# Performance work log

Hardware: AMD Instinct MI355X
Metric: run time of the kernel (lower is better)

Reference implementation:

```python
import jax, jax.numpy as jnp
import numpy as np

HEADS = 8
EMBED = 768
FFN = 4 * EMBED
LN_EPS = 1e-5


def _layernorm(x, g, b):
    m = jnp.mean(x, axis=-1, keepdims=True)
    v = jnp.var(x, axis=-1, keepdims=True)
    return (x - m) * jax.lax.rsqrt(v + LN_EPS) * g + b


def _attention(xn, ctx, Wq, Wkv, Wo, bo, mask):
    # xn: [B, N, C], ctx: [B, M, C], mask: [B, 1, N, M] bool (True = keep)
    B, N, C = xn.shape
    d = C // HEADS
    q = (xn @ Wq).reshape(B, N, HEADS, d).transpose(0, 2, 1, 3)          # b h i d
    k, v = jnp.split(ctx @ Wkv, 2, axis=-1)
    k = k.reshape(B, -1, HEADS, d).transpose(0, 2, 1, 3)                 # b h j d
    v = v.reshape(B, -1, HEADS, d).transpose(0, 2, 1, 3)
    sim = jnp.einsum('bhid,bhjd->bhij', q, k) * (d ** -0.5)
    sim = jnp.where(mask, sim, -jnp.finfo(sim.dtype).max)
    attn = jax.nn.softmax(sim, axis=-1)
    out = jnp.einsum('bhij,bhjd->bhid', attn, v)
    out = out.transpose(0, 2, 1, 3).reshape(B, N, C)
    return out @ Wo + bo


def _block(x, c, effect_lengths, us_rate,
           Wq1, Wkv1, Wo1, bo1, Wq2, Wkv2, Wo2, bo2,
           g1, b1, g2, b2, g4, b4, gc, bc, Wf1, bf1, Wf2, bf2):
    B, L, C = x.shape
    S = c.shape[1]
    el = effect_lengths * us_rate                                        # [B]
    i = jnp.arange(L)
    j_self = jnp.arange(L)
    j_cross = jnp.arange(S)
    # ragged per-sample masks, broadcast over heads: [B, 1, L, L] / [B, 1, L, S]
    mask1 = ((i[None, :, None] < el[:, None, None]) &
             (j_self[None, None, :] < el[:, None, None]))[:, None]
    mask2 = ((i[None, :, None] < el[:, None, None]) &
             (j_cross[None, None, :] < effect_lengths[:, None, None]))[:, None]

    xn = _layernorm(x, g1, b1)
    x = x + _attention(xn, xn, Wq1, Wkv1, Wo1, bo1, mask1)
    xn = _layernorm(x, g2, b2)
    cn = _layernorm(c, gc, bc)
    x = x + _attention(xn, cn, Wq2, Wkv2, Wo2, bo2, mask2)
    xn = _layernorm(x, g4, b4)
    x = x + (jax.nn.gelu(xn @ Wf1 + bf1, approximate=False) @ Wf2 + bf2)
    return x


def setup_inputs() -> dict:
    key = jax.random.key(0)
    ks = jax.random.split(key, 20)
    B, S, US = 8, 512, 2
    L = S * US
    s = 0.02
    inp = {
        'x': jax.random.normal(ks[0], (B, L, EMBED), jnp.float32),
        'c': jax.random.normal(ks[1], (B, S, EMBED), jnp.float32),
        'effect_lengths': jax.random.randint(ks[2], (B,), 1, S + 1),
        'us_rate': US,
        'Wq1': jax.random.normal(ks[3], (EMBED, EMBED), jnp.float32) * s,
        'Wkv1': jax.random.normal(ks[4], (EMBED, 2 * EMBED), jnp.float32) * s,
        'Wo1': jax.random.normal(ks[5], (EMBED, EMBED), jnp.float32) * s,
        'bo1': jnp.zeros((EMBED,), jnp.float32),
        'Wq2': jax.random.normal(ks[6], (EMBED, EMBED), jnp.float32) * s,
        'Wkv2': jax.random.normal(ks[7], (EMBED, 2 * EMBED), jnp.float32) * s,
        'Wo2': jax.random.normal(ks[8], (EMBED, EMBED), jnp.float32) * s,
        'bo2': jnp.zeros((EMBED,), jnp.float32),
        'g1': jnp.ones((EMBED,), jnp.float32), 'b1': jnp.zeros((EMBED,), jnp.float32),
        'g2': jnp.ones((EMBED,), jnp.float32), 'b2': jnp.zeros((EMBED,), jnp.float32),
        'g4': jnp.ones((EMBED,), jnp.float32), 'b4': jnp.zeros((EMBED,), jnp.float32),
        'gc': jnp.ones((EMBED,), jnp.float32), 'bc': jnp.zeros((EMBED,), jnp.float32),
        'Wf1': jax.random.normal(ks[9], (EMBED, FFN), jnp.float32) * s,
        'bf1': jnp.zeros((FFN,), jnp.float32),
        'Wf2': jax.random.normal(ks[10], (FFN, EMBED), jnp.float32) * s,
        'bf2': jnp.zeros((EMBED,), jnp.float32),
    }
    return inp


def reference(x, c, effect_lengths, us_rate,
              Wq1, Wkv1, Wo1, bo1, Wq2, Wkv2, Wo2, bo2,
              g1, b1, g2, b2, g4, b4, gc, bc, Wf1, bf1, Wf2, bf2):
    return _block(x, c, effect_lengths, us_rate,
                  Wq1, Wkv1, Wo1, bo1, Wq2, Wkv2, Wo2, bo2,
                  g1, b1, g2, b2, g4, b4, gc, bc, Wf1, bf1, Wf2, bf2)
```

## Files before the change

kernel.cpp:

```cpp
#include <hip/hip_runtime.h>
#include <math.h>

#define EMBED 768
#define HEADS 8
#define HDIM  96
#define NEG_MASK (-1.0e30f)

typedef unsigned short u16;
typedef unsigned int   u32;

typedef __attribute__((ext_vector_type(4))) float f32x4;
typedef __attribute__((ext_vector_type(8))) short short8;

__device__ __forceinline__ float bf2f(u16 u) {
    return __uint_as_float(((u32)u) << 16);
}
__device__ __forceinline__ u16 f2bf(float f) {
    u32 x = __float_as_uint(f);
    u32 r = (x + 0x7fffu + ((x >> 16) & 1u)) >> 16;
    return (u16)r;
}
__device__ __forceinline__ void unpack2(u32 w, float& lo, float& hi) {
    lo = __uint_as_float(w << 16);
    hi = __uint_as_float(w & 0xffff0000u);
}
__device__ __forceinline__ float wget(const void* p, size_t i, int wf) {
    return wf ? ((const float*)p)[i] : bf2f(((const u16*)p)[i]);
}
__device__ __forceinline__ int bswz(int r, int g) {
    return ((g ^ (r & 3) ^ ((r >> 2) & 3) ^ ((r >> 4) & 3)) << 3);
}

__global__ __launch_bounds__(64) void detect_kernel(const u16* __restrict__ x,
                                                    const int* __restrict__ el,
                                                    const int* __restrict__ usp,
                                                    int* __restrict__ blk) {
    int lane = threadIdx.x;
    int cnt = 0;
    for (int i = lane; i < 4096; i += 64) {
        u32 e = (x[i] >> 7) & 0xFFu;
        if (e >= 0xC0u) cnt++;
    }
#pragma unroll
    for (int off = 32; off > 0; off >>= 1) cnt += __shfl_xor(cnt, off, 64);
    if (lane == 0) {
        blk[0] = (cnt > 32) ? 1 : 0;
        bool i64 = (el[1] == 0) && (el[3] == 0) && (el[5] == 0) && (el[7] == 0);
        for (int b = 0; b < 8; b++) blk[1 + b] = i64 ? el[2 * b] : el[b];
        blk[9] = usp[0];
    }
}

__global__ void wire_to_f32(const void* __restrict__ in, size_t ioff,
                            float* __restrict__ out, int n,
                            const int* __restrict__ blk) {
    int i = blockIdx.x * blockDim.x + threadIdx.x;
    int wf = blk[0];
    if (i < n) out[i] = wget(in, ioff + (size_t)i, wf);
}
__global__ void wire_copy(const void* __restrict__ in, void* __restrict__ out,
                          int n, const int* __restrict__ blk) {
    int i = blockIdx.x * blockDim.x + threadIdx.x;
    int wf = blk[0];
    if (i < n) {
        if (wf) ((float*)out)[i] = ((const float*)in)[i];
        else    ((u16*)out)[i]   = ((const u16*)in)[i];
    }
}
__global__ void f32_to_out(const float* __restrict__ in, void* __restrict__ out,
                           size_t ooff, int n, const int* __restrict__ blk) {
    int i = blockIdx.x * blockDim.x + threadIdx.x;
    int wf = blk[0];
    if (i < n) {
        if (wf) ((float*)out)[ooff + i] = in[i];
        else    ((u16*)out)[ooff + i]   = f2bf(in[i]);
    }
}

__global__ __launch_bounds__(256) void wtrans_kernel(const void* __restrict__ W, size_t woff,
                                                     int ldw, int K,
                                                     u16* __restrict__ WT,
                                                     const int* __restrict__ blk) {
    __shared__ u16 T[64][65];
    int wf = blk[0];
    int n0 = blockIdx.x * 64, k0 = blockIdx.y * 64;
    int tid = threadIdx.x;
    int tr = tid >> 4, tc4 = (tid & 15) * 4;
#pragma unroll
    for (int i = 0; i < 4; i++) {
        int k = tr + i * 16;
        if (wf) {
            const float* src = (const float*)W + woff + (size_t)(k0 + k) * ldw + n0 + tc4;
            float4 f = *(const float4*)src;
            T[tc4 + 0][k] = f2bf(f.x); T[tc4 + 1][k] = f2bf(f.y);
            T[tc4 + 2][k] = f2bf(f.z); T[tc4 + 3][k] = f2bf(f.w);
        } else {
            const u16* src = (const u16*)W + woff + (size_t)(k0 + k) * ldw + n0 + tc4;
            uint2 u = *(const uint2*)src;
            T[tc4 + 0][k] = (u16)(u.x & 0xffffu); T[tc4 + 1][k] = (u16)(u.x >> 16);
            T[tc4 + 2][k] = (u16)(u.y & 0xffffu); T[tc4 + 3][k] = (u16)(u.y >> 16);
        }
    }
    __syncthreads();
#pragma unroll
    for (int i = 0; i < 4; i++) {
        int n = tr + i * 16;
        u32 w0 = (u32)T[n][tc4 + 0] | ((u32)T[n][tc4 + 1] << 16);
        u32 w1 = (u32)T[n][tc4 + 2] | ((u32)T[n][tc4 + 3] << 16);
        *(uint2*)(WT + (size_t)(n0 + n) * K + k0 + tc4) = make_uint2(w0, w1);
    }
}

__global__ __launch_bounds__(256) void ln_kernel(const void* __restrict__ in,
                                                 size_t ioff, int sel,
                                                 const void* __restrict__ g,
                                                 const void* __restrict__ b,
                                                 u16* __restrict__ out,
                                                 const int* __restrict__ blk) {
    int wf = blk[0];
    int row = blockIdx.x, tid = threadIdx.x;
    size_t base = ioff + (size_t)row * EMBED;
    float v[3];
#pragma unroll
    for (int e = 0; e < 3; e++) {
        size_t idx = base + tid + e * 256;
        v[e] = (sel == 0) ? ((const float*)in)[idx] : wget(in, idx, wf);
    }
    float s = v[0] + v[1] + v[2];
    float q = v[0] * v[0] + v[1] * v[1] + v[2] * v[2];
#pragma unroll
    for (int off = 32; off > 0; off >>= 1) {
        s += __shfl_xor(s, off, 64);
        q += __shfl_xor(q, off, 64);
    }
    __shared__ float sb[8];
    int wid = tid >> 6, lane = tid & 63;
    if (lane == 0) { sb[wid] = s; sb[4 + wid] = q; }
    __syncthreads();
    if (tid == 0) {
        sb[0] = sb[0] + sb[1] + sb[2] + sb[3];
        sb[4] = sb[4] + sb[5] + sb[6] + sb[7];
    }
    __syncthreads();
    float mean = sb[0] * (1.0f / EMBED);
    float var  = sb[4] * (1.0f / EMBED) - mean * mean;
    float rs   = rsqrtf(var + 1e-5f);
    size_t obase = (size_t)row * EMBED;
#pragma unroll
    for (int e = 0; e < 3; e++) {
        int col = tid + e * 256;
        out[obase + col] = f2bf((v[e] - mean) * rs * wget(g, col, wf) + wget(b, col, wf));
    }
}

__global__ __launch_bounds__(256) void gemm_kernel(const u16* __restrict__ A,
                                                   const void* __restrict__ W,
                                                   size_t woff, int ldw,
                                                   const void* __restrict__ bias, int boff,
                                                   void* __restrict__ Cv, size_t coff,
                                                   int M, int N, int K, int flags,
                                                   int tcmode, const int* __restrict__ blk) {
    __shared__ float As[16][64];
    __shared__ float Bs[16][64];
    int wf = blk[0];
    int tid = threadIdx.x;
    int tx = tid & 15, ty = tid >> 4;
    int row0 = blockIdx.y * 64, col0 = blockIdx.x * 64;
    float acc[4][4] = {};
    int ar = tid >> 2, ac4 = tid & 3;
    int br = tid >> 4, bc4 = tid & 15;

    for (int kb = 0; kb < K; kb += 16) {
        {
            uint2 u = *(const uint2*)(A + (size_t)(row0 + ar) * K + kb + ac4 * 4);
            float a0, a1, a2, a3;
            unpack2(u.x, a0, a1); unpack2(u.y, a2, a3);
            As[ac4 * 4 + 0][ar] = a0; As[ac4 * 4 + 1][ar] = a1;
            As[ac4 * 4 + 2][ar] = a2; As[ac4 * 4 + 3][ar] = a3;
        }
        {
            size_t off = woff + (size_t)(kb + br) * ldw + col0 + bc4 * 4;
            if (wf) {
                float4 u = *(const float4*)((const float*)W + off);
                Bs[br][bc4 * 4 + 0] = u.x; Bs[br][bc4 * 4 + 1] = u.y;
                Bs[br][bc4 * 4 + 2] = u.z; Bs[br][bc4 * 4 + 3] = u.w;
            } else {
                uint2 u = *(const uint2*)((const u16*)W + off);
                float b0, b1, b2, b3;
                unpack2(u.x, b0, b1); unpack2(u.y, b2, b3);
                Bs[br][bc4 * 4 + 0] = b0; Bs[br][bc4 * 4 + 1] = b1;
                Bs[br][bc4 * 4 + 2] = b2; Bs[br][bc4 * 4 + 3] = b3;
            }
        }
        __syncthreads();
#pragma unroll
        for (int kk = 0; kk < 16; kk++) {
            float4 a = *(const float4*)&As[kk][ty * 4];
            float4 b = *(const float4*)&Bs[kk][tx * 4];
            float av[4] = {a.x, a.y, a.z, a.w};
            float bv[4] = {b.x, b.y, b.z, b.w};
#pragma unroll
            for (int i = 0; i < 4; i++)
#pragma unroll
                for (int j = 0; j < 4; j++)
                    acc[i][j] += av[i] * bv[j];
        }
        __syncthreads();
    }

#pragma unroll
    for (int i = 0; i < 4; i++) {
        int m = row0 + ty * 4 + i;
#pragma unroll
        for (int j = 0; j < 4; j++) {
            int n = col0 + tx * 4 + j;
            float v = acc[i][j];
            if (flags & 1) v += wget(bias, boff + n, wf);
            if (flags & 2) v = 0.5f * v * (1.0f + erff(v * 0.70710678118654752f));
            size_t idx = coff + (size_t)m * N + n;
            if (tcmode == 0) {
                ((float*)Cv)[idx] += v;
            } else if (tcmode == 1) {
                ((u16*)Cv)[idx] = f2bf(v);
            } else {
                if (wf) ((float*)Cv)[idx] += v;
                else { u16* p = (u16*)Cv; p[idx] = f2bf(v + bf2f(p[idx])); }
            }
        }
    }
}

__global__ __launch_bounds__(256) void gemm_mfma(const u16* __restrict__ A,
                                                 const void* __restrict__ W,
                                                 size_t woff, int ldw,
                                                 const void* __restrict__ bias, int boff,
                                                 void* __restrict__ Cv, size_t coff,
                                                 int M, int N, int K, int flags,
                                                 int tcmode, const int* __restrict__ blk) {
    __shared__ __align__(16) u16 As[128 * 32];
    __shared__ __align__(16) u16 Bs[128 * 32];
    int wf = blk[0];
    int tid = threadIdx.x;
    int wave = tid >> 6, lane = tid & 63;
    int x = lane & 15, g = lane >> 4;
    int wm = wave >> 1, wn = wave & 1;
    int row0 = blockIdx.y * 128, col0 = blockIdx.x * 128;

    int ar  = tid >> 1, ah = tid & 1;
    int bk  = tid >> 3, bn0 = (tid & 7) * 16;

    f32x4 acc[4][4];
#pragma unroll
    for (int i = 0; i < 4; i++)
#pragma unroll
        for (int j = 0; j < 4; j++) acc[i][j] = (f32x4){0.f, 0.f, 0.f, 0.f};

    for (int kb = 0; kb < K; kb += 32) {
        {
            const u16* asrc = A + (size_t)(row0 + ar) * K + kb + ah * 16;
            uint4 a0 = *(const uint4*)asrc;
            uint4 a1 = *(const uint4*)(asrc + 8);
            *(uint4*)&As[ar * 32 + bswz(ar, ah * 2 + 0)] = a0;
            *(uint4*)&As[ar * 32 + bswz(ar, ah * 2 + 1)] = a1;
        }
        {
            u16 bv[16];
            if (wf) {
                const float* wsrc = (const float*)W + woff + (size_t)(kb + bk) * ldw + col0 + bn0;
#pragma unroll
                for (int i = 0; i < 16; i += 4) {
                    float4 f = *(const float4*)(wsrc + i);
                    bv[i + 0] = f2bf(f.x); bv[i + 1] = f2bf(f.y);
                    bv[i + 2] = f2bf(f.z); bv[i + 3] = f2bf(f.w);
                }
            } else {
                const u16* wsrc = (const u16*)W + woff + (size_t)(kb + bk) * ldw + col0 + bn0;
                ((uint4*)bv)[0] = *(const uint4*)wsrc;
                ((uint4*)bv)[1] = *(const uint4*)(wsrc + 8);
            }
            int kg = bk >> 3, kl = bk & 7;
#pragma unroll
            for (int i = 0; i < 16; i++)
                Bs[(bn0 + i) * 32 + bswz(bn0 + i, kg) + kl] = bv[i];
        }
        __syncthreads();

        short8 af[4], bf[4];
#pragma unroll
        for (int mt = 0; mt < 4; mt++) {
            int r = wm * 64 + mt * 16 + x;
            af[mt] = *(const short8*)&As[r * 32 + bswz(r, g)];
        }
#pragma unroll
        for (int nt = 0; nt < 4; nt++) {
            int n = wn * 64 + nt * 16 + x;
            bf[nt] = *(const short8*)&Bs[n * 32 + bswz(n, g)];
        }
#pragma unroll
        for (int mt = 0; mt < 4; mt++)
#pragma unroll
            for (int nt = 0; nt < 4; nt++)
                acc[mt][nt] = __builtin_amdgcn_mfma_f32_16x16x32_bf16(af[mt], bf[nt], acc[mt][nt], 0, 0, 0);
        __syncthreads();
    }

#pragma unroll
    for (int mt = 0; mt < 4; mt++) {
#pragma unroll
        for (int nt = 0; nt < 4; nt++) {
#pragma unroll
            for (int r = 0; r < 4; r++) {
                int m = row0 + wm * 64 + mt * 16 + g * 4 + r;
                int n = col0 + wn * 64 + nt * 16 + x;
                float v = acc[mt][nt][r];
                if (flags & 1) v += wget(bias, boff + n, wf);
                if (flags & 2) v = 0.5f * v * (1.0f + erff(v * 0.70710678118654752f));
                size_t idx = coff + (size_t)m * N + n;
                if (tcmode == 0) {
                    ((float*)Cv)[idx] += v;
                } else if (tcmode == 1) {
                    ((u16*)Cv)[idx] = f2bf(v);
                } else {
                    if (wf) ((float*)Cv)[idx] += v;
                    else { u16* p = (u16*)Cv; p[idx] = f2bf(v + bf2f(p[idx])); }
                }
            }
        }
    }
}

__global__ __launch_bounds__(256) void gemm_mfma_t(const u16* __restrict__ A,
                                                   const u16* __restrict__ BT,
                                                   const void* __restrict__ bias, int boff,
                                                   void* __restrict__ Cv, size_t coff,
                                                   int M, int N, int K, int flags,
                                                   int tcmode, const int* __restrict__ blk) {
    __shared__ __align__(16) u16 As[2][128 * 32];
    __shared__ __align__(16) u16 Bs[2][128 * 32];
    int wf = blk[0];
    int tid = threadIdx.x;
    int wave = tid >> 6, lane = tid & 63;
    int x = lane & 15, g = lane >> 4;
    int wm = wave >> 1, wn = wave & 1;
    int row0 = blockIdx.y * 128, col0 = blockIdx.x * 128;
    int KS = gridDim.z, kz = blockIdx.z;
    int Kc = K / KS;

    int sr = tid >> 1;
    int sg = (tid & 1) * 2;
    const u16* aptr = A  + (size_t)(row0 + sr) * K + kz * Kc + sg * 8;
    const u16* bptr = BT + (size_t)(col0 + sr) * K + kz * Kc + sg * 8;
    int wo0 = sr * 32 + bswz(sr, sg);
    int wo1 = sr * 32 + bswz(sr, sg + 1);

    int ra[4], rb[4];
#pragma unroll
    for (int t = 0; t < 4; t++) {
        int r = wm * 64 + t * 16 + x;
        int n = wn * 64 + t * 16 + x;
        ra[t] = r * 32 + bswz(r, g);
        rb[t] = n * 32 + bswz(n, g);
    }

    f32x4 acc[4][4];
#pragma unroll
    for (int i = 0; i < 4; i++)
#pragma unroll
        for (int j = 0; j < 4; j++) acc[i][j] = (f32x4){0.f, 0.f, 0.f, 0.f};

    int nsteps = Kc >> 5;

    {
        uint4 a0 = *(const uint4*)aptr, a1 = *(const uint4*)(aptr + 8);
        uint4 b0 = *(const uint4*)bptr, b1 = *(const uint4*)(bptr + 8);
        *(uint4*)&As[0][wo0] = a0; *(uint4*)&As[0][wo1] = a1;
        *(uint4*)&Bs[0][wo0] = b0; *(uint4*)&Bs[0][wo1] = b1;
    }
    uint4 s0a0 = {}, s0a1 = {}, s0b0 = {}, s0b1 = {};
    uint4 s1a0 = {}, s1a1 = {}, s1b0 = {}, s1b1 = {};
    if (nsteps > 1) {
        aptr += 32; bptr += 32;
        s1a0 = *(const uint4*)aptr; s1a1 = *(const uint4*)(aptr + 8);
        s1b0 = *(const uint4*)bptr; s1b1 = *(const uint4*)(bptr + 8);
    }
    __syncthreads();

#define GSTEP(S, LA0, LA1, LB0, LB1, WA0, WA1, WB0, WB1)                          \
    {                                                                             \
        if ((S) + 2 < nsteps) {                                                   \
            aptr += 32; bptr += 32;                                               \
            LA0 = *(const uint4*)aptr; LA1 = *(const uint4*)(aptr + 8);           \
            LB0 = *(const uint4*)bptr; LB1 = *(const uint4*)(bptr + 8);           \
        }                                                                         \
        short8 af[4], bfr[4];                                                     \
        _Pragma("unroll")                                                         \
        for (int mt = 0; mt < 4; mt++)                                            \
            af[mt] = *(const short8*)&As[(S) & 1][ra[mt]];                        \
        _Pragma("unroll")                                                         \
        for (int nt = 0; nt < 4; nt++)                                            \
            bfr[nt] = *(const short8*)&Bs[(S) & 1][rb[nt]];                       \
        _Pragma("unroll")                                                         \
        for (int mt = 0; mt < 4; mt++)                                            \
            _Pragma("unroll")                                                     \
            for (int nt = 0; nt < 4; nt++)                                        \
                acc[mt][nt] = __builtin_amdgcn_mfma_f32_16x16x32_bf16(            \
                    af[mt], bfr[nt], acc[mt][nt], 0, 0, 0);                       \
        if ((S) + 1 < nsteps) {                                                   \
            int nb = (((S) & 1) ^ 1);                                             \
            *(uint4*)&As[nb][wo0] = WA0; *(uint4*)&As[nb][wo1] = WA1;             \
            *(uint4*)&Bs[nb][wo0] = WB0; *(uint4*)&Bs[nb][wo1] = WB1;             \
            __syncthreads();                                                      \
        }                                                                         \
    }

    for (int s = 0; s < nsteps; s += 2) {
        GSTEP(s, s0a0, s0a1, s0b0, s0b1, s1a0, s1a1, s1b0, s1b1);
        if (s + 1 < nsteps)
            GSTEP(s + 1, s1a0, s1a1, s1b0, s1b1, s0a0, s0a1, s0b0, s0b1);
    }
#undef GSTEP

    bool kz0 = (kz == 0);
#pragma unroll
    for (int mt = 0; mt < 4; mt++) {
#pragma unroll
        for (int nt = 0; nt < 4; nt++) {
#pragma unroll
            for (int r = 0; r < 4; r++) {
                int m = row0 + wm * 64 + mt * 16 + g * 4 + r;
                int n = col0 + wn * 64 + nt * 16 + x;
                float v = acc[mt][nt][r];
                if ((flags & 1) && kz0) v += wget(bias, boff + n, wf);
                if (flags & 2) v = 0.5f * v * (1.0f + erff(v * 0.70710678118654752f));
                size_t idx = coff + (size_t)m * N + n;
                if (tcmode == 0) {
                    if (KS > 1) atomicAdd(&((float*)Cv)[idx], v);
                    else        ((float*)Cv)[idx] += v;
                } else if (tcmode == 1) {
                    ((u16*)Cv)[idx] = f2bf(v);
                } else {
                    if (wf) ((float*)Cv)[idx] += v;
                    else { u16* p = (u16*)Cv; p[idx] = f2bf(v + bf2f(p[idx])); }
                }
            }
        }
    }
}

__global__ __launch_bounds__(256) void attn_kernel(const u16* __restrict__ Q,
                                                   const u16* __restrict__ K,
                                                   const u16* __restrict__ V,
                                                   u16* __restrict__ AO,
                                                   int ldq, int ldk, int ldv, int ldo,
                                                   size_t qss, size_t kss, size_t oss,
                                                   const int* __restrict__ blk,
                                                   int bfix, int Lk, int is_self) {
    int bz   = (bfix < 0) ? blockIdx.z : 0;
    int bidx = (bfix < 0) ? blockIdx.z : bfix;
    const u16* Qp = Q + (size_t)bz * qss;
    const u16* Kp = K + (size_t)bz * kss;
    const u16* Vp = V + (size_t)bz * kss;
    u16* AOp = AO + (size_t)bz * oss;

    int hoff = blockIdx.y * HDIM;
    int i0 = blockIdx.x * 64;
    int tid = threadIdx.x;
    int wave = tid >> 6, lane = tid & 63;
    int x = lane & 15, g = lane >> 4;

    int elb = blk[1 + bidx];
    int el_q = elb * blk[9];
    int el_k = is_self ? el_q : elb;

    __shared__ __align__(16) u16 Ks[64 * 96];
    __shared__ __align__(16) u16 Vs[96 * 64];
    __shared__ __align__(16) u16 Ps[4][16 * 72];

    short8 qf[3];
    {
        const u16* qrow = Qp + (size_t)(i0 + wave * 16 + x) * ldq + hoff;
#pragma unroll
        for (int kc = 0; kc < 3; kc++)
            qf[kc] = *(const short8*)(qrow + kc * 32 + g * 8);
    }

    const f32x4 zero4 = {0.f, 0.f, 0.f, 0.f};
    f32x4 o[6];
#pragma unroll
    for (int dt = 0; dt < 6; dt++) o[dt] = zero4;
    float m[4], l[4];
#pragma unroll
    for (int r = 0; r < 4; r++) { m[r] = NEG_MASK; l[r] = 0.f; }

    bool qok[4];
#pragma unroll
    for (int r = 0; r < 4; r++) qok[r] = (i0 + wave * 16 + g * 4 + r) < el_q;

    const float scale = 0.10206207261596576f;
    u16* pw = &Ps[wave][0];

    for (int kt0 = 0; kt0 < Lk; kt0 += 64) {
#pragma unroll
        for (int t = 0; t < 3; t++) {
            int idx = tid + t * 256;
            int j = idx / 12, c = idx % 12;
            *(uint4*)&Ks[j * 96 + c * 8] =
                *(const uint4*)(Kp + (size_t)(kt0 + j) * ldk + hoff + c * 8);
            uint4 vu = *(const uint4*)(Vp + (size_t)(kt0 + j) * ldv + hoff + c * 8);
            u16 vv[8] = {(u16)(vu.x & 0xffffu), (u16)(vu.x >> 16),
                         (u16)(vu.y & 0xffffu), (u16)(vu.y >> 16),
                         (u16)(vu.z & 0xffffu), (u16)(vu.z >> 16),
                         (u16)(vu.w & 0xffffu), (u16)(vu.w >> 16)};
            int jb = j >> 3, jl = j & 7;
#pragma unroll
            for (int ii = 0; ii < 8; ii++) {
                int d = c * 8 + ii;
                int sb = jb ^ (d & 7) ^ ((d >> 3) & 7);
                Vs[d * 64 + sb * 8 + jl] = vv[ii];
            }
        }
        __syncthreads();

        f32x4 st[4];
#pragma unroll
        for (int t = 0; t < 4; t++) {
            f32x4 acc = zero4;
#pragma unroll
            for (int kc = 0; kc < 3; kc++) {
                short8 kf = *(const short8*)&Ks[(t * 16 + x) * 96 + kc * 32 + g * 8];
                acc = __builtin_amdgcn_mfma_f32_16x16x32_bf16(qf[kc], kf, acc, 0, 0, 0);
            }
            st[t] = acc;
        }

#pragma unroll
        for (int t = 0; t < 4; t++) {
            bool kv_ok = (kt0 + t * 16 + x) < el_k;
#pragma unroll
            for (int r = 0; r < 4; r++)
                st[t][r] = (kv_ok && qok[r]) ? st[t][r] * scale : NEG_MASK;
        }

        float al[4];
#pragma unroll
        for (int r = 0; r < 4; r++) {
            float rm = fmaxf(fmaxf(st[0][r], st[1][r]), fmaxf(st[2][r], st[3][r]));
            rm = fmaxf(rm, __shfl_xor(rm, 1, 64));
            rm = fmaxf(rm, __shfl_xor(rm, 2, 64));
            rm = fmaxf(rm, __shfl_xor(rm, 4, 64));
            rm = fmaxf(rm, __shfl_xor(rm, 8, 64));
            float mn = fmaxf(m[r], rm);
            al[r] = __expf(m[r] - mn);
            m[r] = mn;
            l[r] *= al[r];
        }
#pragma unroll
        for (int dt = 0; dt < 6; dt++)
#pragma unroll
            for (int r = 0; r < 4; r++) o[dt][r] *= al[r];

#pragma unroll
        for (int t = 0; t < 4; t++)
#pragma unroll
            for (int r = 0; r < 4; r++) {
                float p = __expf(st[t][r] - m[r]);
                l[r] += p;
                pw[(g * 4 + r) * 72 + t * 16 + x] = f2bf(p);
            }

#pragma unroll
        for (int kc = 0; kc < 2; kc++) {
            short8 pf = *(const short8*)&pw[x * 72 + kc * 32 + g * 8];
#pragma unroll
            for (int dt = 0; dt < 6; dt++) {
                int d = dt * 16 + x;
                int sb = (kc * 4 + g) ^ (d & 7) ^ ((d >> 3) & 7);
                short8 vf = *(const short8*)&Vs[d * 64 + sb * 8];
                o[dt] = __builtin_amdgcn_mfma_f32_16x16x32_bf16(pf, vf, o[dt], 0, 0, 0);
            }
        }
        __syncthreads();
    }

    float inv[4];
#pragma unroll
    for (int r = 0; r < 4; r++) {
        float lr = l[r];
        lr += __shfl_xor(lr, 1, 64);
        lr += __shfl_xor(lr, 2, 64);
        lr += __shfl_xor(lr, 4, 64);
        lr += __shfl_xor(lr, 8, 64);
        inv[r] = 1.0f / lr;
    }
#pragma unroll
    for (int dt = 0; dt < 6; dt++)
#pragma unroll
        for (int r = 0; r < 4; r++) {
            size_t ob = (size_t)(i0 + wave * 16 + g * 4 + r) * ldo + hoff + dt * 16 + x;
            AOp[ob] = f2bf(o[dt][r] * inv[r]);
        }
}

extern "C" void kernel_launch(void* const* d_in, const int* in_sizes, int n_in,
                              void* d_out, int out_size, void* d_ws, size_t ws_size,
                              hipStream_t stream) {
    const void* x    = d_in[0];
    const void* c    = d_in[1];
    const int* el    = (const int*)d_in[2];
    const int* us    = (const int*)d_in[3];
    const void* Wq1  = d_in[4];
    const void* Wkv1 = d_in[5];
    const void* Wo1  = d_in[6];
    const void* bo1  = d_in[7];
    const void* Wq2  = d_in[8];
    const void* Wkv2 = d_in[9];
    const void* Wo2  = d_in[10];
    const void* bo2  = d_in[11];
    const void* g1 = d_in[12]; const void* b1 = d_in[13];
    const void* g2 = d_in[14]; const void* b2 = d_in[15];
    const void* g4 = d_in[16]; const void* b4 = d_in[17];
    const void* gc = d_in[18]; const void* bc = d_in[19];
    const void* Wf1 = d_in[20]; const void* bf1 = d_in[21];
    const void* Wf2 = d_in[22]; const void* bf2 = d_in[23];

    const int B = 8, S = 512, L = 1024, C = EMBED;
    const int NX = B * L * C;
    const size_t RL = (size_t)L * C;
    const size_t RS = (size_t)S * C;

    char* ws = (char*)d_ws;
    int*  blk = (int*)ws;
    dim3 blkd(256);

    bool tierA = ws_size >= (size_t)88080448;
    bool tierB = !tierA && ws_size >= (size_t)33030208;

    detect_kernel<<<1, 64, 0, stream>>>((const u16*)x, el, us, blk);

    if (tierA) {
        float* X  = (float*)(ws + 64);
        u16*   XN = (u16*)(ws + 25165888);
        u16*   WT = (u16*)(ws + 37748800);
        char*  P  = ws + 47185984;
        u16* Qb   = (u16*)P;
        u16* KVb  = (u16*)(P + 12582912);
        u16* CNb  = (u16*)P;
        u16* KV2b = (u16*)(P + 6291456);
        u16* Q2b  = (u16*)(P + 18874368);
        u16* Hh   = (u16*)P;
        const size_t WTq = 0, WTkv = 589824, WTo = 1769472;
        const size_t WTf1 = 0, WTf2 = 2359296;

        wire_to_f32<<<(NX + 255) / 256, blkd, 0, stream>>>(x, 0, X, NX, blk);

        wtrans_kernel<<<dim3(12, 12), blkd, 0, stream>>>(Wq1, 0, C, C, WT + WTq, blk);
        wtrans_kernel<<<dim3(24, 12), blkd, 0, stream>>>(Wkv1, 0, 2 * C, C, WT + WTkv, blk);
        wtrans_kernel<<<dim3(12, 12), blkd, 0, stream>>>(Wo1, 0, C, C, WT + WTo, blk);

        ln_kernel<<<B * L, blkd, 0, stream>>>(X, 0, 0, g1, b1, XN, blk);
        gemm_mfma_t<<<dim3(6, 64, 1), blkd, 0, stream>>>(XN, WT + WTq, nullptr, 0, Qb, 0, B * L, C, C, 0, 1, blk);
        gemm_mfma_t<<<dim3(12, 64, 1), blkd, 0, stream>>>(XN, WT + WTkv, nullptr, 0, KVb, 0, B * L, 2 * C, C, 0, 1, blk);
        attn_kernel<<<dim3(16, 8, 8), blkd, 0, stream>>>(Qb, KVb, KVb + C, Qb, C, 2 * C, 2 * C, C,
                                                         RL, (size_t)L * 2 * C, RL, blk, -1, L, 1);
        gemm_mfma_t<<<dim3(6, 64, 2), blkd, 0, stream>>>(Qb, WT + WTo, bo1, 0, X, 0, B * L, C, C, 1, 0, blk);

        wtrans_kernel<<<dim3(12, 12), blkd, 0, stream>>>(Wq2, 0, C, C, WT + WTq, blk);
        wtrans_kernel<<<dim3(24, 12), blkd, 0, stream>>>(Wkv2, 0, 2 * C, C, WT + WTkv, blk);
        wtrans_kernel<<<dim3(12, 12), blkd, 0, stream>>>(Wo2, 0, C, C, WT + WTo, blk);

        ln_kernel<<<B * L, blkd, 0, stream>>>(X, 0, 0, g2, b2, XN, blk);
        ln_kernel<<<B * S, blkd, 0, stream>>>(c, 0, 2, gc, bc, CNb, blk);
        gemm_mfma_t<<<dim3(12, 32, 1), blkd, 0, stream>>>(CNb, WT + WTkv, nullptr, 0, KV2b, 0, B * S, 2 * C, C, 0, 1, blk);
        gemm_mfma_t<<<dim3(6, 64, 1), blkd, 0, stream>>>(XN, WT + WTq, nullptr, 0, Q2b, 0, B * L, C, C, 0, 1, blk);
        attn_kernel<<<dim3(16, 8, 8), blkd, 0, stream>>>(Q2b, KV2b, KV2b + C, Q2b, C, 2 * C, 2 * C, C,
                                                         RL, (size_t)S * 2 * C, RL, blk, -1, S, 0);
        gemm_mfma_t<<<dim3(6, 64, 2), blkd, 0, stream>>>(Q2b, WT + WTo, bo2, 0, X, 0, B * L, C, C, 1, 0, blk);

        wtrans_kernel<<<dim3(48, 12), blkd, 0, stream>>>(Wf1, 0, 4 * C, C, WT + WTf1, blk);
        wtrans_kernel<<<dim3(12, 48), blkd, 0, stream>>>(Wf2, 0, C, 4 * C, WT + WTf2, blk);

        ln_kernel<<<B * L, blkd, 0, stream>>>(X, 0, 0, g4, b4, XN, blk);
        for (int h = 0; h < 2; h++) {
            size_t ro = (size_t)h * 4096 * C;
            gemm_mfma_t<<<dim3(24, 32, 1), blkd, 0, stream>>>(XN + ro, WT + WTf1, bf1, 0, Hh, 0, 4096, 4 * C, C, 1 | 2, 1, blk);
            gemm_mfma_t<<<dim3(6, 32, 2), blkd, 0, stream>>>(Hh, WT + WTf2, bf2, 0, X, ro, 4096, C, 4 * C, 1, 0, blk);
        }

        f32_to_out<<<(NX + 255) / 256, blkd, 0, stream>>>(X, d_out, 0, NX, blk);
    } else if (tierB) {
        float* X  = (float*)(ws + 64);
        u16*   XN = (u16*)(ws + 64 + 25165824);
        char*  P  = ws + 64 + 25165824 + 1572864;
        u16* Qb   = (u16*)P;
        u16* KVb  = (u16*)(P + 1572864);
        u16* AOb  = (u16*)(P + 4718592);
        u16* CNb  = (u16*)P;
        u16* KV2b = (u16*)(P + 786432);
        u16* Q2b  = (u16*)(P + 2359296);
        u16* AO2b = (u16*)(P + 3932160);
        u16* Hb   = (u16*)P;

        wire_to_f32<<<(NX + 255) / 256, blkd, 0, stream>>>(x, 0, X, NX, blk);

        for (int b = 0; b < B; b++) {
            size_t ro = (size_t)b * RL;
            ln_kernel<<<L, blkd, 0, stream>>>(X, ro, 0, g1, b1, XN, blk);
            gemm_mfma<<<dim3(6, 8), blkd, 0, stream>>>(XN, Wq1, 0, C, nullptr, 0, Qb, 0, L, C, C, 0, 1, blk);
            gemm_mfma<<<dim3(12, 8), blkd, 0, stream>>>(XN, Wkv1, 0, 2 * C, nullptr, 0, KVb, 0, L, 2 * C, C, 0, 1, blk);
            attn_kernel<<<dim3(16, 8), blkd, 0, stream>>>(Qb, KVb, KVb + C, AOb, C, 2 * C, 2 * C, C, 0, 0, 0, blk, b, L, 1);
            gemm_mfma<<<dim3(6, 8), blkd, 0, stream>>>(AOb, Wo1, 0, C, bo1, 0, X, ro, L, C, C, 1, 0, blk);

            ln_kernel<<<L, blkd, 0, stream>>>(X, ro, 0, g2, b2, XN, blk);
            ln_kernel<<<S, blkd, 0, stream>>>(c, (size_t)b * RS, 2, gc, bc, CNb, blk);
            gemm_mfma<<<dim3(12, 4), blkd, 0, stream>>>(CNb, Wkv2, 0, 2 * C, nullptr, 0, KV2b, 0, S, 2 * C, C, 0, 1, blk);
            gemm_mfma<<<dim3(6, 8), blkd, 0, stream>>>(XN, Wq2, 0, C, nullptr, 0, Q2b, 0, L, C, C, 0, 1, blk);
            attn_kernel<<<dim3(16, 8), blkd, 0, stream>>>(Q2b, KV2b, KV2b + C, AO2b, C, 2 * C, 2 * C, C, 0, 0, 0, blk, b, S, 0);
            gemm_mfma<<<dim3(6, 8), blkd, 0, stream>>>(AO2b, Wo2, 0, C, bo2, 0, X, ro, L, C, C, 1, 0, blk);

            ln_kernel<<<L, blkd, 0, stream>>>(X, ro, 0, g4, b4, XN, blk);
            gemm_mfma<<<dim3(24, 8), blkd, 0, stream>>>(XN, Wf1, 0, 4 * C, bf1, 0, Hb, 0, L, 4 * C, C, 1 | 2, 1, blk);
            gemm_mfma<<<dim3(6, 8), blkd, 0, stream>>>(Hb, Wf2, 0, C, bf2, 0, X, ro, L, C, 4 * C, 1, 0, blk);
        }
        f32_to_out<<<(NX + 255) / 256, blkd, 0, stream>>>(X, d_out, 0, NX, blk);
    } else {
        u16*  XN  = (u16*)(ws + 64);
        u16*  CNb = (u16*)(ws + 64 + 1572864);
        char* P2  = ws + 64 + 1572864 + 786432;
        u16* Qp  = (u16*)P2;
        u16* Kp  = (u16*)(P2 + 393216);
        u16* Vp  = (u16*)(P2 + 786432);
        u16* AOp = (u16*)(P2 + 1179648);
        u16* Hc  = (u16*)P2;

        wire_copy<<<(NX + 255) / 256, blkd, 0, stream>>>(x, d_out, NX, blk);

        for (int b = 0; b < B; b++) {
            size_t ro = (size_t)b * RL;

            ln_kernel<<<L, blkd, 0, stream>>>(d_out, ro, 2, g1, b1, XN, blk);
            for (int p = 0; p < 4; p++) {
                int h = 2 * p;
                gemm_kernel<<<dim3(3, 16), blkd, 0, stream>>>(XN, Wq1, (size_t)h * 96, C, nullptr, 0, Qp, 0, L, 192, C, 0, 1, blk);
                gemm_kernel<<<dim3(3, 16), blkd, 0, stream>>>(XN, Wkv1, (size_t)h * 96, 2 * C, nullptr, 0, Kp, 0, L, 192, C, 0, 1, blk);
                gemm_kernel<<<dim3(3, 16), blkd, 0, stream>>>(XN, Wkv1, (size_t)(C + h * 96), 2 * C, nullptr, 0, Vp, 0, L, 192, C, 0, 1, blk);
                attn_kernel<<<dim3(16, 2), blkd, 0, stream>>>(Qp, Kp, Vp, AOp, 192, 192, 192, 192, 0, 0, 0, blk, b, L, 1);
                gemm_kernel<<<dim3(12, 16), blkd, 0, stream>>>(AOp, Wo1, (size_t)h * 96 * C, C, bo1, 0, d_out, ro, L, C, 192, (p == 0) ? 1 : 0, 3, blk);
            }
            ln_kernel<<<L, blkd, 0, stream>>>(d_out, ro, 2, g2, b2, XN, blk);
            ln_kernel<<<S, blkd, 0, stream>>>(c, (size_t)b * RS, 2, gc, bc, CNb, blk);
            for (int p = 0; p < 4; p++) {
                int h = 2 * p;
                gemm_kernel<<<dim3(3, 16), blkd, 0, stream>>>(XN, Wq2, (size_t)h * 96, C, nullptr, 0, Qp, 0, L, 192, C, 0, 1, blk);
                gemm_kernel<<<dim3(3, 8), blkd, 0, stream>>>(CNb, Wkv2, (size_t)h * 96, 2 * C, nullptr, 0, Kp, 0, S, 192, C, 0, 1, blk);
                gemm_kernel<<<dim3(3, 8), blkd, 0, stream>>>(CNb, Wkv2, (size_t)(C + h * 96), 2 * C, nullptr, 0, Vp, 0, S, 192, C, 0, 1, blk);
                attn_kernel<<<dim3(16, 2), blkd, 0, stream>>>(Qp, Kp, Vp, AOp, 192, 192, 192, 192, 0, 0, 0, blk, b, S, 0);
                gemm_kernel<<<dim3(12, 16), blkd, 0, stream>>>(AOp, Wo2, (size_t)h * 96 * C, C, bo2, 0, d_out, ro, L, C, 192, (p == 0) ? 1 : 0, 3, blk);
            }
            ln_kernel<<<L, blkd, 0, stream>>>(d_out, ro, 2, g4, b4, XN, blk);
            for (int ch = 0; ch < 4; ch++) {
                gemm_kernel<<<dim3(12, 16), blkd, 0, stream>>>(XN, Wf1, (size_t)ch * C, 4 * C, bf1, ch * C, Hc, 0, L, C, C, 1 | 2, 1, blk);
                gemm_kernel<<<dim3(12, 16), blkd, 0, stream>>>(Hc, Wf2, (size_t)ch * C * C, C, bf2, 0, d_out, ro, L, C, C, (ch == 0) ? 1 : 0, 3, blk);
            }
        }
    }
}
```

Baseline: 924.0 us.

## Shrink GEMM M-tile to 64, add LDS-only barrier, skip masked attention tiles

The MFMA GEMM tile shrinks from 128x128 to 64x128, doubling the grid for better CU occupancy, and the out-projection GEMMs drop split-K. The __syncthreads is replaced by a barrier that waits only on LDS counters, so in-flight global prefetches are not drained. The attention kernel trims the key loop to the valid effective length for fully valid query tiles, and skips QK loads and MFMAs for fully masked query tiles while keeping the V path. These cut wasted compute on masked regions and improve GEMM parallelism, at the cost of lower per-block reuse in the GEMM.

After: 850.8 us. 7.9% less time.

```diff
diff --git a/kernel.cpp b/kernel.cpp
--- a/kernel.cpp
+++ b/kernel.cpp
@@ -29,6 +29,12 @@
 }
 __device__ __forceinline__ int bswz(int r, int g) {
     return ((g ^ (r & 3) ^ ((r >> 2) & 3) ^ ((r >> 4) & 3)) << 3);
+}
+__device__ __forceinline__ void lds_barrier() {
+    __builtin_amdgcn_sched_barrier(0);
+    asm volatile("s_waitcnt lgkmcnt(0)" ::: "memory");
+    __builtin_amdgcn_s_barrier();
+    __builtin_amdgcn_sched_barrier(0);
 }
 
 __global__ __launch_bounds__(64) void detect_kernel(const u16* __restrict__ x,
@@ -335,99 +341,100 @@
                                                    void* __restrict__ Cv, size_t coff,
                                                    int M, int N, int K, int flags,
                                                    int tcmode, const int* __restrict__ blk) {
-    __shared__ __align__(16) u16 As[2][128 * 32];
+    __shared__ __align__(16) u16 As[2][64 * 32];
     __shared__ __align__(16) u16 Bs[2][128 * 32];
     int wf = blk[0];
     int tid = threadIdx.x;
     int wave = tid >> 6, lane = tid & 63;
     int x = lane & 15, g = lane >> 4;
     int wm = wave >> 1, wn = wave & 1;
-    int row0 = blockIdx.y * 128, col0 = blockIdx.x * 128;
+    int row0 = blockIdx.y * 64, col0 = blockIdx.x * 128;
     int KS = gridDim.z, kz = blockIdx.z;
     int Kc = K / KS;
 
-    int sr = tid >> 1;
-    int sg = (tid & 1) * 2;
-    const u16* aptr = A  + (size_t)(row0 + sr) * K + kz * Kc + sg * 8;
-    const u16* bptr = BT + (size_t)(col0 + sr) * K + kz * Kc + sg * 8;
-    int wo0 = sr * 32 + bswz(sr, sg);
-    int wo1 = sr * 32 + bswz(sr, sg + 1);
-
-    int ra[4], rb[4];
-#pragma unroll
-    for (int t = 0; t < 4; t++) {
-        int r = wm * 64 + t * 16 + x;
-        int n = wn * 64 + t * 16 + x;
-        ra[t] = r * 32 + bswz(r, g);
-        rb[t] = n * 32 + bswz(n, g);
-    }
-
-    f32x4 acc[4][4];
-#pragma unroll
-    for (int i = 0; i < 4; i++)
+    int ar = tid >> 2, ac = tid & 3;
+    const u16* aptr = A + (size_t)(row0 + ar) * K + kz * Kc + ac * 8;
+    int awo = ar * 32 + bswz(ar, ac);
+    int br = tid >> 1, bh = tid & 1;
+    const u16* bptr = BT + (size_t)(col0 + br) * K + kz * Kc + bh * 16;
+    int bwo0 = br * 32 + bswz(br, 2 * bh);
+    int bwo1 = br * 32 + bswz(br, 2 * bh + 1);
+
+    int ra[2], rb[4];
+#pragma unroll
+    for (int mt = 0; mt < 2; mt++) {
+        int r = wm * 32 + mt * 16 + x;
+        ra[mt] = r * 32 + bswz(r, g);
+    }
+#pragma unroll
+    for (int nt = 0; nt < 4; nt++) {
+        int n = wn * 64 + nt * 16 + x;
+        rb[nt] = n * 32 + bswz(n, g);
+    }
+
+    f32x4 acc[2][4];
+#pragma unroll
+    for (int i = 0; i < 2; i++)
 #pragma unroll
         for (int j = 0; j < 4; j++) acc[i][j] = (f32x4){0.f, 0.f, 0.f, 0.f};
 
     int nsteps = Kc >> 5;
 
-    {
-        uint4 a0 = *(const uint4*)aptr, a1 = *(const uint4*)(aptr + 8);
-        uint4 b0 = *(const uint4*)bptr, b1 = *(const uint4*)(bptr + 8);
-        *(uint4*)&As[0][wo0] = a0; *(uint4*)&As[0][wo1] = a1;
-        *(uint4*)&Bs[0][wo0] = b0; *(uint4*)&Bs[0][wo1] = b1;
-    }
-    uint4 s0a0 = {}, s0a1 = {}, s0b0 = {}, s0b1 = {};
-    uint4 s1a0 = {}, s1a1 = {}, s1b0 = {}, s1b1 = {};
+    *(uint4*)&As[0][awo]  = *(const uint4*)aptr;
+    *(uint4*)&Bs[0][bwo0] = *(const uint4*)bptr;
+    *(uint4*)&Bs[0][bwo1] = *(const uint4*)(bptr + 8);
+    uint4 s0a = {}, s0b0 = {}, s0b1 = {};
+    uint4 s1a = {}, s1b0 = {}, s1b1 = {};
     if (nsteps > 1) {
         aptr += 32; bptr += 32;
-        s1a0 = *(const uint4*)aptr; s1a1 = *(const uint4*)(aptr + 8);
+        s1a  = *(const uint4*)aptr;
         s1b0 = *(const uint4*)bptr; s1b1 = *(const uint4*)(bptr + 8);
     }
-    __syncthreads();
-
-#define GSTEP(S, LA0, LA1, LB0, LB1, WA0, WA1, WB0, WB1)                          \
+    lds_barrier();
+
+#define GSTEP(S, LA, LB0, LB1, WA, WB0, WB1)                                      \
     {                                                                             \
         if ((S) + 2 < nsteps) {                                                   \
             aptr += 32; bptr += 32;                                               \
-            LA0 = *(const uint4*)aptr; LA1 = *(const uint4*)(aptr + 8);           \
+            LA  = *(const uint4*)aptr;                                            \
             LB0 = *(const uint4*)bptr; LB1 = *(const uint4*)(bptr + 8);           \
         }                                                                         \
-        short8 af[4], bfr[4];                                                     \
+        short8 af[2], bfr[4];                                                     \
         _Pragma("unroll")                                                         \
-        for (int mt = 0; mt < 4; mt++)                                            \
+        for (int mt = 0; mt < 2; mt++)                                            \
             af[mt] = *(const short8*)&As[(S) & 1][ra[mt]];                        \
         _Pragma("unroll")                                                         \
         for (int nt = 0; nt < 4; nt++)                                            \
             bfr[nt] = *(const short8*)&Bs[(S) & 1][rb[nt]];                       \
         _Pragma("unroll")                                                         \
-        for (int mt = 0; mt < 4; mt++)                                            \
+        for (int mt = 0; mt < 2; mt++)                                            \
             _Pragma("unroll")                                                     \
             for (int nt = 0; nt < 4; nt++)                                        \
                 acc[mt][nt] = __builtin_amdgcn_mfma_f32_16x16x32_bf16(            \
                     af[mt], bfr[nt], acc[mt][nt], 0, 0, 0);                       \
         if ((S) + 1 < nsteps) {                                                   \
             int nb = (((S) & 1) ^ 1);                                             \
-            *(uint4*)&As[nb][wo0] = WA0; *(uint4*)&As[nb][wo1] = WA1;             \
-            *(uint4*)&Bs[nb][wo0] = WB0; *(uint4*)&Bs[nb][wo1] = WB1;             \
-            __syncthreads();                                                      \
+            *(uint4*)&As[nb][awo]  = WA;                                          \
+            *(uint4*)&Bs[nb][bwo0] = WB0; *(uint4*)&Bs[nb][bwo1] = WB1;           \
+            lds_barrier();                                                        \
         }                                                                         \
     }
 
     for (int s = 0; s < nsteps; s += 2) {
-        GSTEP(s, s0a0, s0a1, s0b0, s0b1, s1a0, s1a1, s1b0, s1b1);
+        GSTEP(s, s0a, s0b0, s0b1, s1a, s1b0, s1b1);
         if (s + 1 < nsteps)
-            GSTEP(s + 1, s1a0, s1a1, s1b0, s1b1, s0a0, s0a1, s0b0, s0b1);
+            GSTEP(s + 1, s1a, s1b0, s1b1, s0a, s0b0, s0b1);
     }
 #undef GSTEP
 
     bool kz0 = (kz == 0);
 #pragma unroll
-    for (int mt = 0; mt < 4; mt++) {
+    for (int mt = 0; mt < 2; mt++) {
 #pragma unroll
         for (int nt = 0; nt < 4; nt++) {
 #pragma unroll
             for (int r = 0; r < 4; r++) {
-                int m = row0 + wm * 64 + mt * 16 + g * 4 + r;
+                int m = row0 + wm * 32 + mt * 16 + g * 4 + r;
                 int n = col0 + wn * 64 + nt * 16 + x;
                 float v = acc[mt][nt][r];
                 if ((flags & 1) && kz0) v += wget(bias, boff + n, wf);
@@ -472,6 +479,13 @@
     int el_q = elb * blk[9];
     int el_k = is_self ? el_q : elb;
 
+    bool allinv = (i0 >= el_q);
+    int Lk_loop = Lk;
+    if (!allinv && (i0 + 64 <= el_q)) {
+        int lke = (el_k + 63) & ~63;
+        Lk_loop = (lke < Lk) ? lke : Lk;
+    }
+
     __shared__ __align__(16) u16 Ks[64 * 96];
     __shared__ __align__(16) u16 Vs[96 * 64];
     __shared__ __align__(16) u16 Ps[4][16 * 72];
@@ -499,13 +513,15 @@
     const float scale = 0.10206207261596576f;
     u16* pw = &Ps[wave][0];
 
-    for (int kt0 = 0; kt0 < Lk; kt0 += 64) {
+    for (int kt0 = 0; kt0 < Lk_loop; kt0 += 64) {
 #pragma unroll
         for (int t = 0; t < 3; t++) {
             int idx = tid + t * 256;
             int j = idx / 12, c = idx % 12;
-            *(uint4*)&Ks[j * 96 + c * 8] =
-                *(const uint4*)(Kp + (size_t)(kt0 + j) * ldk + hoff + c * 8);
+            if (!allinv) {
+                *(uint4*)&Ks[j * 96 + c * 8] =
+                    *(const uint4*)(Kp + (size_t)(kt0 + j) * ldk + hoff + c * 8);
+            }
             uint4 vu = *(const uint4*)(Vp + (size_t)(kt0 + j) * ldv + hoff + c * 8);
             u16 vv[8] = {(u16)(vu.x & 0xffffu), (u16)(vu.x >> 16),
                          (u16)(vu.y & 0xffffu), (u16)(vu.y >> 16),
@@ -522,15 +538,20 @@
         __syncthreads();
 
         f32x4 st[4];
-#pragma unroll
-        for (int t = 0; t < 4; t++) {
-            f32x4 acc = zero4;
-#pragma unroll
-            for (int kc = 0; kc < 3; kc++) {
-                short8 kf = *(const short8*)&Ks[(t * 16 + x) * 96 + kc * 32 + g * 8];
-                acc = __builtin_amdgcn_mfma_f32_16x16x32_bf16(qf[kc], kf, acc, 0, 0, 0);
-            }
-            st[t] = acc;
+        if (!allinv) {
+#pragma unroll
+            for (int t = 0; t < 4; t++) {
+                f32x4 acc = zero4;
+#pragma unroll
+                for (int kc = 0; kc < 3; kc++) {
+                    short8 kf = *(const short8*)&Ks[(t * 16 + x) * 96 + kc * 32 + g * 8];
+                    acc = __builtin_amdgcn_mfma_f32_16x16x32_bf16(qf[kc], kf, acc, 0, 0, 0);
+                }
+                st[t] = acc;
+            }
+        } else {
+#pragma unroll
+            for (int t = 0; t < 4; t++) st[t] = zero4;
         }
 
 #pragma unroll
@@ -658,11 +679,11 @@
         wtrans_kernel<<<dim3(12, 12), blkd, 0, stream>>>(Wo1, 0, C, C, WT + WTo, blk);
 
         ln_kernel<<<B * L, blkd, 0, stream>>>(X, 0, 0, g1, b1, XN, blk);
-        gemm_mfma_t<<<dim3(6, 64, 1), blkd, 0, stream>>>(XN, WT + WTq, nullptr, 0, Qb, 0, B * L, C, C, 0, 1, blk);
-        gemm_mfma_t<<<dim3(12, 64, 1), blkd, 0, stream>>>(XN, WT + WTkv, nullptr, 0, KVb, 0, B * L, 2 * C, C, 0, 1, blk);
+        gemm_mfma_t<<<dim3(6, 128, 1), blkd, 0, stream>>>(XN, WT + WTq, nullptr, 0, Qb, 0, B * L, C, C, 0, 1, blk);
+        gemm_mfma_t<<<dim3(12, 128, 1), blkd, 0, stream>>>(XN, WT + WTkv, nullptr, 0, KVb, 0, B * L, 2 * C, C, 0, 1, blk);
         attn_kernel<<<dim3(16, 8, 8), blkd, 0, stream>>>(Qb, KVb, KVb + C, Qb, C, 2 * C, 2 * C, C,
                                                          RL, (size_t)L * 2 * C, RL, blk, -1, L, 1);
-        gemm_mfma_t<<<dim3(6, 64, 2), blkd, 0, stream>>>(Qb, WT + WTo, bo1, 0, X, 0, B * L, C, C, 1, 0, blk);
+        gemm_mfma_t<<<dim3(6, 128, 1), blkd, 0, stream>>>(Qb, WT + WTo, bo1, 0, X, 0, B * L, C, C, 1, 0, blk);
 
         wtrans_kernel<<<dim3(12, 12), blkd, 0, stream>>>(Wq2, 0, C, C, WT + WTq, blk);
         wtrans_kernel<<<dim3(24, 12), blkd, 0, stream>>>(Wkv2, 0, 2 * C, C, WT + WTkv, blk);
@@ -670,11 +691,11 @@
 
         ln_kernel<<<B * L, blkd, 0, stream>>>(X, 0, 0, g2, b2, XN, blk);
         ln_kernel<<<B * S, blkd, 0, stream>>>(c, 0, 2, gc, bc, CNb, blk);
-        gemm_mfma_t<<<dim3(12, 32, 1), blkd, 0, stream>>>(CNb, WT + WTkv, nullptr, 0, KV2b, 0, B * S, 2 * C, C, 0, 1, blk);
-        gemm_mfma_t<<<dim3(6, 64, 1), blkd, 0, stream>>>(XN, WT + WTq, nullptr, 0, Q2b, 0, B * L, C, C, 0, 1, blk);
+        gemm_mfma_t<<<dim3(12, 64, 1), blkd, 0, stream>>>(CNb, WT + WTkv, nullptr, 0, KV2b, 0, B * S, 2 * C, C, 0, 1, blk);
+        gemm_mfma_t<<<dim3(6, 128, 1), blkd, 0, stream>>>(XN, WT + WTq, nullptr, 0, Q2b, 0, B * L, C, C, 0, 1, blk);
         attn_kernel<<<dim3(16, 8, 8), blkd, 0, stream>>>(Q2b, KV2b, KV2b + C, Q2b, C, 2 * C, 2 * C, C,
                                                          RL, (size_t)S * 2 * C, RL, blk, -1, S, 0);
-        gemm_mfma_t<<<dim3(6, 64, 2), blkd, 0, stream>>>(Q2b, WT + WTo, bo2, 0, X, 0, B * L, C, C, 1, 0, blk);
+        gemm_mfma_t<<<dim3(6, 128, 1), blkd, 0, stream>>>(Q2b, WT + WTo, bo2, 0, X, 0, B * L, C, C, 1, 0, blk);
 
         wtrans_kernel<<<dim3(48, 12), blkd, 0, stream>>>(Wf1, 0, 4 * C, C, WT + WTf1, blk);
         wtrans_kernel<<<dim3(12, 48), blkd, 0, stream>>>(Wf2, 0, C, 4 * C, WT + WTf2, blk);
@@ -682,8 +703,8 @@
         ln_kernel<<<B * L, blkd, 0, stream>>>(X, 0, 0, g4, b4, XN, blk);
         for (int h = 0; h < 2; h++) {
             size_t ro = (size_t)h * 4096 * C;
-            gemm_mfma_t<<<dim3(24, 32, 1), blkd, 0, stream>>>(XN + ro, WT + WTf1, bf1, 0, Hh, 0, 4096, 4 * C, C, 1 | 2, 1, blk);
-            gemm_mfma_t<<<dim3(6, 32, 2), blkd, 0, stream>>>(Hh, WT + WTf2, bf2, 0, X, ro, 4096, C, 4 * C, 1, 0, blk);
+            gemm_mfma_t<<<dim3(24, 64, 1), blkd, 0, stream>>>(XN + ro, WT + WTf1, bf1, 0, Hh, 0, 4096, 4 * C, C, 1 | 2, 1, blk);
+            gemm_mfma_t<<<dim3(6, 64, 2), blkd, 0, stream>>>(Hh, WT + WTf2, bf2, 0, X, ro, 4096, C, 4 * C, 1, 0, blk);
         }
 
         f32_to_out<<<(NX + 255) / 256, blkd, 0, stream>>>(X, d_out, 0, NX, blk);
```
